# Kernel optimization log

Hardware: AMD Instinct MI355X
Metric: run time of the kernel (lower is better)

The kernel has to match this reference:

```python
import jax, jax.numpy as jnp
import numpy as np

B, S, D = 8, 4096, 768
HEADS = 12
NEIGHBORS = 2
DILATION = 1
KERNEL = 1 + 2 * NEIGHBORS  # 5
DIM_HEAD = D // HEADS


def setup_inputs() -> dict:
    key = jax.random.key(0)
    ks = jax.random.split(key, 11)
    sc = 1.0 / np.sqrt(D)
    return {
        "x": jax.random.normal(ks[0], (B, S, D), dtype=jnp.float32),
        "Wq": jax.random.normal(ks[1], (D, D), dtype=jnp.float32) * sc,
        "bq": jax.random.normal(ks[2], (D,), dtype=jnp.float32) * 0.02,
        "Wk": jax.random.normal(ks[3], (D, D), dtype=jnp.float32) * sc,
        "bk": jax.random.normal(ks[4], (D,), dtype=jnp.float32) * 0.02,
        "Wv": jax.random.normal(ks[5], (D, D), dtype=jnp.float32) * sc,
        "bv": jax.random.normal(ks[6], (D,), dtype=jnp.float32) * 0.02,
        "Wo": jax.random.normal(ks[7], (D, D), dtype=jnp.float32) * sc,
        "bo": jax.random.normal(ks[8], (D,), dtype=jnp.float32) * 0.02,
        "gamma": jnp.ones((D,), dtype=jnp.float32),
        "beta": jnp.zeros((D,), dtype=jnp.float32),
    }


def _extract_seq_patches(x, kernel_size, dilation):
    # [B, S, D] -> [B, S, kernel_size, D] of dilated local windows, zero-padded.
    seq_len = x.shape[1]
    patch_size = kernel_size + (dilation - 1) * (kernel_size - 1)
    pad_r = (patch_size - 1) // 2
    pad_l = patch_size - pad_r - 1
    xp = jnp.pad(x, ((0, 0), (pad_l, pad_r), (0, 0)))
    # small fixed loop over kernel positions (kernel_size = 5)
    return jnp.stack([xp[:, i:i + seq_len] for i in range(0, patch_size, dilation)], axis=2)


def reference(x, Wq, bq, Wk, bk, Wv, bv, Wo, bo, gamma, beta):
    patches = _extract_seq_patches(x, KERNEL, DILATION)  # [B, S, K, D]
    q = x @ Wq + bq                                       # [B, S, D]
    k = patches @ Wk + bk                                 # [B, S, K, D]
    v = patches @ Wv + bv                                 # [B, S, K, D]
    # split heads
    q = q.reshape(B, S, HEADS, DIM_HEAD)
    k = k.reshape(B, S, KERNEL, HEADS, DIM_HEAD)
    v = v.reshape(B, S, KERNEL, HEADS, DIM_HEAD)
    scale = jnp.sqrt(jnp.asarray(DIM_HEAD, dtype=q.dtype))
    scores = jnp.einsum('bshd,bskhd->bshk', q, k) / scale  # [B, S, H, K]
    p = jax.nn.softmax(scores, axis=-1)
    att = jnp.einsum('bshk,bskhd->bshd', p, v)             # [B, S, H, dh]
    att = att.reshape(B, S, D)
    att = att @ Wo + bo
    y = att + x
    # LayerNorm over last dim
    mu = jnp.mean(y, axis=-1, keepdims=True)
    var = jnp.var(y, axis=-1, keepdims=True)
    y = (y - mu) / jnp.sqrt(var + 1e-5) * gamma + beta
    return y
```

## Files before the change

### kernel.cpp

```cpp
#include <hip/hip_runtime.h>

#define B_  8
#define S_  4096
#define D_  768
#define H_  12
#define M_  (B_ * S_)
#define NQKV_ 2304
#define NTILES 12

typedef unsigned short u16;
typedef __attribute__((ext_vector_type(4))) float  f32x4;
typedef __attribute__((ext_vector_type(8))) __bf16 bf16x8;
typedef __attribute__((ext_vector_type(4))) u16    u16x4;

#define GAS __attribute__((address_space(1)))
#define LAS __attribute__((address_space(3)))

__device__ __forceinline__ u16 f2bf(float f) {
    unsigned u = __float_as_uint(f);
    u += 0x7FFF + ((u >> 16) & 1);
    return (u16)(u >> 16);
}
__device__ __forceinline__ float bf2f(u16 h) {
    return __uint_as_float(((unsigned)h) << 16);
}

__device__ __forceinline__ void gload_lds16(const void* g, void* l) {
    __builtin_amdgcn_global_load_lds((const GAS void*)g, (LAS void*)l, 16, 0, 0);
}

__device__ __forceinline__ int xcd_swz(int bid, int nwg) {
    return (bid & 7) * (nwg >> 3) + (bid >> 3);
}

__global__ __launch_bounds__(256) void castx_kernel(const float* __restrict__ x,
                                                    u16* __restrict__ xb) {
    const int i = blockIdx.x * 256 + threadIdx.x;
    const float4 v = ((const float4*)x)[i];
    u16x4 o;
    o.x = f2bf(v.x); o.y = f2bf(v.y); o.z = f2bf(v.z); o.w = f2bf(v.w);
    ((u16x4*)xb)[i] = o;
}

__global__ __launch_bounds__(256) void wtrans_kernel(const float* __restrict__ Wq,
                                                     const float* __restrict__ Wk,
                                                     const float* __restrict__ Wv,
                                                     const float* __restrict__ Wo,
                                                     u16* __restrict__ Wb) {
    const float* W = (blockIdx.z == 0) ? Wq : (blockIdx.z == 1) ? Wk
                   : (blockIdx.z == 2) ? Wv : Wo;
    u16* O = Wb + (size_t)blockIdx.z * D_ * D_;
    __shared__ float tile[32][33];
    const int tx = threadIdx.x & 31, ty = threadIdx.x >> 5;
    const int k0 = blockIdx.y * 32, n0 = blockIdx.x * 32;
#pragma unroll
    for (int j = 0; j < 4; j++)
        tile[ty + j * 8][tx] = W[(size_t)(k0 + ty + j * 8) * D_ + n0 + tx];
    __syncthreads();
#pragma unroll
    for (int j = 0; j < 4; j++)
        O[(size_t)(n0 + ty + j * 8) * D_ + k0 + tx] = f2bf(tile[tx][ty + j * 8]);
}


#define MFMA16(AF, BF)                                                       \
    __builtin_amdgcn_s_setprio(1);                                           \
    _Pragma("unroll") for (int mi = 0; mi < 4; ++mi)                         \
        _Pragma("unroll") for (int ni = 0; ni < 4; ++ni)                     \
            acc[mi][ni] = __builtin_amdgcn_mfma_f32_16x16x32_bf16(           \
                AF[mi], BF[ni], acc[mi][ni], 0, 0, 0);                       \
    __builtin_amdgcn_s_setprio(0)

#define RD(p, imm) (*(const bf16x8*)((p) + (imm)))

template <int MODE>
__global__ __launch_bounds__(256, 2) void gemm2_kernel(
    const u16* __restrict__ A, const u16* __restrict__ Wb,
    const float* __restrict__ b0, const float* __restrict__ b1,
    const float* __restrict__ b2,
    u16* __restrict__ outb, const u16* __restrict__ xres) {
    extern __shared__ char lds[];

    const int t = threadIdx.x;
    const int w = t >> 6, l = t & 63;
    const int wm = w >> 1, wn = w & 1;

    const int NTN = (MODE == 0) ? 18 : 6;
    const int work = xcd_swz(blockIdx.x, gridDim.x);
    const int mt = work / NTN, nt = work % NTN;
    const int m0 = mt * 128;
    const int col0 = nt * 128;
    const int widx = (MODE == 0) ? (nt / 6) : 3;
    const int n0w  = (MODE == 0) ? (nt % 6) * 128 : col0;

    const int srow = w * 32 + (l >> 3);
    const int schunk = (l & 7) ^ ((l >> 3) & 7);
    const u16* Asrc = A + (size_t)(m0 + srow) * D_ + schunk * 8;
    const u16* Bsrc = Wb + (size_t)widx * (D_ * D_)
                         + (size_t)(n0w + srow) * D_ + schunk * 8;
    char* const dstA = lds + w * 4096;
    char* const dstB = lds + 16384 + w * 4096;

    const int ck0 = (((l >> 4) ^ (l & 7)) << 4);
    const int ck1 = ((((l >> 4) + 4) ^ (l & 7)) << 4);
    const char* aB = lds + (wm * 64 + (l & 15)) * 128;
    const char* bB = lds + 16384 + (wn * 64 + (l & 15)) * 128;

    f32x4 acc[4][4];
#pragma unroll
    for (int i = 0; i < 4; i++)
#pragma unroll
        for (int j = 0; j < 4; j++) acc[i][j] = (f32x4){0.f, 0.f, 0.f, 0.f};

    auto STAGE = [&](int tk, int b) {
        const int ko = tk * 64;
        char* da = dstA + b * 32768;
        char* db = dstB + b * 32768;
#pragma unroll
        for (int g = 0; g < 4; ++g) {
            gload_lds16(Asrc + ko + g * 8 * D_, da + g * 1024);
            gload_lds16(Bsrc + ko + g * 8 * D_, db + g * 1024);
        }
    };

    STAGE(0, 0);
    __syncthreads();

#pragma unroll
    for (int X = 0; X < NTILES; ++X) {
        const int cb = (X & 1) * 32768;
        if (X + 1 < NTILES) STAGE(X + 1, (X & 1) ^ 1);

        bf16x8 af[4], bf[4];
#pragma unroll
        for (int mi = 0; mi < 4; ++mi) af[mi] = RD(aB, cb + mi * 2048 + ck0);
#pragma unroll
        for (int ni = 0; ni < 4; ++ni) bf[ni] = RD(bB, cb + ni * 2048 + ck0);
        MFMA16(af, bf);
#pragma unroll
        for (int mi = 0; mi < 4; ++mi) af[mi] = RD(aB, cb + mi * 2048 + ck1);
#pragma unroll
        for (int ni = 0; ni < 4; ++ni) bf[ni] = RD(bB, cb + ni * 2048 + ck1);
        MFMA16(af, bf);

        __syncthreads();
    }

    const int crow0 = m0 + wm * 64 + ((l >> 4) << 2);
    const int ccol0 = col0 + wn * 64 + (l & 15);
    if (MODE == 0) {
        const float* bias = (widx == 0) ? b0 : (widx == 1) ? b1 : b2;
        const int bcol0 = ccol0 - widx * D_;
#pragma unroll
        for (int mi = 0; mi < 4; ++mi)
#pragma unroll
            for (int ni = 0; ni < 4; ++ni) {
                const float bv = bias[bcol0 + ni * 16];
#pragma unroll
                for (int r = 0; r < 4; ++r)
                    outb[(size_t)(crow0 + mi * 16 + r) * NQKV_ + ccol0 + ni * 16] =
                        f2bf(acc[mi][ni][r] + bv);
            }
    } else {
#pragma unroll
        for (int mi = 0; mi < 4; ++mi)
#pragma unroll
            for (int ni = 0; ni < 4; ++ni) {
                const int col = ccol0 + ni * 16;
                const float bv = b0[col];
#pragma unroll
                for (int r = 0; r < 4; ++r) {
                    const size_t idx = (size_t)(crow0 + mi * 16 + r) * D_ + col;
                    outb[idx] = f2bf(acc[mi][ni][r] + bv + bf2f(xres[idx]));
                }
            }
    }
}

__global__ __launch_bounds__(256) void attn_kernel(const u16* __restrict__ QKV,
                                                   const float* __restrict__ bk,
                                                   const float* __restrict__ bv,
                                                   u16* __restrict__ att) {
    const int gw = xcd_swz(blockIdx.x, gridDim.x) * 4 + (threadIdx.x >> 6);
    const int l  = threadIdx.x & 63;
    const int hq = gw % 3;
    const int m  = gw / 3;
    const int s  = m & (S_ - 1);
    const int col = hq * 256 + l * 4;
    const u16* base = QKV + (size_t)m * NQKV_;

    const u16x4 qv = *(const u16x4*)(base + col);
    float qf[4];
#pragma unroll
    for (int j = 0; j < 4; j++) qf[j] = bf2f(qv[j]);

    float sc[5];
#pragma unroll
    for (int i = 0; i < 5; i++) {
        const int sp = s + i - 2;
        float p;
        if (sp >= 0 && sp < S_) {
            const u16x4 kv = *(const u16x4*)(base + (i - 2) * NQKV_ + D_ + col);
            p = qf[0] * bf2f(kv[0]) + qf[1] * bf2f(kv[1])
              + qf[2] * bf2f(kv[2]) + qf[3] * bf2f(kv[3]);
        } else {
            const float4 kb = *(const float4*)(bk + col);
            p = qf[0] * kb.x + qf[1] * kb.y + qf[2] * kb.z + qf[3] * kb.w;
        }
#pragma unroll
        for (int off = 1; off < 16; off <<= 1) p += __shfl_xor(p, off, 64);
        sc[i] = p * 0.125f;
    }
    float mx = sc[0];
#pragma unroll
    for (int i = 1; i < 5; i++) mx = fmaxf(mx, sc[i]);
    float e[5], sum = 0.f;
#pragma unroll
    for (int i = 0; i < 5; i++) { e[i] = __expf(sc[i] - mx); sum += e[i]; }
    const float inv = 1.f / sum;

    float o[4] = {0.f, 0.f, 0.f, 0.f};
#pragma unroll
    for (int i = 0; i < 5; i++) {
        const float wgt = e[i] * inv;
        const int sp = s + i - 2;
        if (sp >= 0 && sp < S_) {
            const u16x4 vv = *(const u16x4*)(base + (i - 2) * NQKV_ + 2 * D_ + col);
#pragma unroll
            for (int j = 0; j < 4; j++) o[j] += wgt * bf2f(vv[j]);
        } else {
            const float4 vb = *(const float4*)(bv + col);
            o[0] += wgt * vb.x; o[1] += wgt * vb.y;
            o[2] += wgt * vb.z; o[3] += wgt * vb.w;
        }
    }
    u16x4 ov;
#pragma unroll
    for (int j = 0; j < 4; j++) ov[j] = f2bf(o[j]);
    *(u16x4*)(att + (size_t)m * D_ + col) = ov;
}

__global__ __launch_bounds__(256) void ln_kernel(const u16* __restrict__ Yb,
                                                 const float* __restrict__ gamma,
                                                 const float* __restrict__ beta,
                                                 float* __restrict__ out) {
    const int row = blockIdx.x;
    const u16* r = Yb + (size_t)row * D_;
    const int t = threadIdx.x;
    const float v0 = bf2f(r[t]), v1 = bf2f(r[t + 256]), v2 = bf2f(r[t + 512]);
    float s  = v0 + v1 + v2;
    float s2 = v0 * v0 + v1 * v1 + v2 * v2;
#pragma unroll
    for (int off = 32; off > 0; off >>= 1) {
        s  += __shfl_xor(s,  off, 64);
        s2 += __shfl_xor(s2, off, 64);
    }
    __shared__ float red[8];
    const int w = t >> 6, l = t & 63;
    if (l == 0) { red[w] = s; red[4 + w] = s2; }
    __syncthreads();
    s  = red[0] + red[1] + red[2] + red[3];
    s2 = red[4] + red[5] + red[6] + red[7];
    const float mu  = s * (1.f / 768.f);
    const float var = s2 * (1.f / 768.f) - mu * mu;
    const float inv = rsqrtf(var + 1e-5f);
    float* o = out + (size_t)row * D_;
    o[t]       = (v0 - mu) * inv * gamma[t]       + beta[t];
    o[t + 256] = (v1 - mu) * inv * gamma[t + 256] + beta[t + 256];
    o[t + 512] = (v2 - mu) * inv * gamma[t + 512] + beta[t + 512];
}

extern "C" void kernel_launch(void* const* d_in, const int* in_sizes, int n_in,
                              void* d_out, int out_size, void* d_ws, size_t ws_size,
                              hipStream_t stream) {
    const float* x     = (const float*)d_in[0];
    const float* Wq    = (const float*)d_in[1];
    const float* bq    = (const float*)d_in[2];
    const float* Wk    = (const float*)d_in[3];
    const float* bk    = (const float*)d_in[4];
    const float* Wv    = (const float*)d_in[5];
    const float* bv    = (const float*)d_in[6];
    const float* Wo    = (const float*)d_in[7];
    const float* bo    = (const float*)d_in[8];
    const float* gamma = (const float*)d_in[9];
    const float* beta  = (const float*)d_in[10];

    char* ws = (char*)d_ws;
    u16*   Wb  = (u16*)ws;
    u16*   xb  = (u16*)(ws + 4718592);
    u16*   QKV = (u16*)(ws + 4718592 + 50331648);
    u16*   yb  = QKV;
    u16*   att = (u16*)d_out;

    (void)hipFuncSetAttribute(reinterpret_cast<const void*>(&gemm2_kernel<0>),
                              hipFuncAttributeMaxDynamicSharedMemorySize, 65536);
    (void)hipFuncSetAttribute(reinterpret_cast<const void*>(&gemm2_kernel<1>),
                              hipFuncAttributeMaxDynamicSharedMemorySize, 65536);

    castx_kernel<<<(M_ * D_) / (256 * 4), 256, 0, stream>>>(x, xb);
    wtrans_kernel<<<dim3(24, 24, 4), 256, 0, stream>>>(Wq, Wk, Wv, Wo, Wb);
    gemm2_kernel<0><<<(M_ / 128) * 18, 256, 65536, stream>>>(xb, Wb, bq, bk, bv,
                                                             QKV, nullptr);
    attn_kernel<<<(M_ * 3) / 4, 256, 0, stream>>>(QKV, bk, bv, att);
    gemm2_kernel<1><<<(M_ / 128) * 6, 256, 65536, stream>>>(att, Wb, bo, nullptr, nullptr,
                                                            yb, xb);
    ln_kernel<<<M_, 256, 0, stream>>>(yb, gamma, beta, (float*)d_out);
}
```

Before: 291.8 us.

## Replace LDS-staged GEMM with register-direct global loads and 64x64 per-wave tiles

Both GEMMs stop staging A and B tiles through double-buffered LDS with global_load_lds. Each wave now loads its MFMA fragments straight from global memory into registers, using two register buffers that alternate. The block tile changes from 128x128 (2x2 waves) to 64x256: each wave owns a 64x64 output tile and shares the A rows with the other waves only through cache. This removes LDS traffic and block barriers, but gives up cross-wave reuse, so global and L2 traffic per FLOP goes up and register pressure rises.

```diff
diff --git a/kernel.cpp b/kernel.cpp
--- a/kernel.cpp
+++ b/kernel.cpp
@@ -13,9 +13,6 @@
 typedef __attribute__((ext_vector_type(8))) __bf16 bf16x8;
 typedef __attribute__((ext_vector_type(4))) u16    u16x4;
 
-#define GAS __attribute__((address_space(1)))
-#define LAS __attribute__((address_space(3)))
-
 __device__ __forceinline__ u16 f2bf(float f) {
     unsigned u = __float_as_uint(f);
     u += 0x7FFF + ((u >> 16) & 1);
@@ -23,10 +20,6 @@
 }
 __device__ __forceinline__ float bf2f(u16 h) {
     return __uint_as_float(((unsigned)h) << 16);
-}
-
-__device__ __forceinline__ void gload_lds16(const void* g, void* l) {
-    __builtin_amdgcn_global_load_lds((const GAS void*)g, (LAS void*)l, 16, 0, 0);
 }
 
 __device__ __forceinline__ int xcd_swz(int bid, int nwg) {
@@ -63,48 +56,48 @@
 }
 
 
-#define MFMA16(AF, BF)                                                       \
+#define RDG(p, off) (*(const bf16x8*)((p) + (off)))
+
+#define LOADT(FA, FB, kt)                                                    \
+    _Pragma("unroll") for (int mi = 0; mi < 4; ++mi)                         \
+        _Pragma("unroll") for (int kh = 0; kh < 2; ++kh)                     \
+            FA[mi][kh] = RDG(Ap, (size_t)mi * 16 * D_ + (kt) * 64 + kh * 32); \
+    _Pragma("unroll") for (int ni = 0; ni < 4; ++ni)                         \
+        _Pragma("unroll") for (int kh = 0; kh < 2; ++kh)                     \
+            FB[ni][kh] = RDG(Bp, (size_t)ni * 16 * D_ + (kt) * 64 + kh * 32)
+
+#define MFMA_ALL(FA, FB)                                                     \
     __builtin_amdgcn_s_setprio(1);                                           \
-    _Pragma("unroll") for (int mi = 0; mi < 4; ++mi)                         \
-        _Pragma("unroll") for (int ni = 0; ni < 4; ++ni)                     \
-            acc[mi][ni] = __builtin_amdgcn_mfma_f32_16x16x32_bf16(           \
-                AF[mi], BF[ni], acc[mi][ni], 0, 0, 0);                       \
+    _Pragma("unroll") for (int kh = 0; kh < 2; ++kh)                         \
+        _Pragma("unroll") for (int mi = 0; mi < 4; ++mi)                     \
+            _Pragma("unroll") for (int ni = 0; ni < 4; ++ni)                 \
+                acc[mi][ni] = __builtin_amdgcn_mfma_f32_16x16x32_bf16(       \
+                    FA[mi][kh], FB[ni][kh], acc[mi][ni], 0, 0, 0);           \
     __builtin_amdgcn_s_setprio(0)
 
-#define RD(p, imm) (*(const bf16x8*)((p) + (imm)))
-
 template <int MODE>
-__global__ __launch_bounds__(256, 2) void gemm2_kernel(
+__global__ __launch_bounds__(256) void gemmr_kernel(
     const u16* __restrict__ A, const u16* __restrict__ Wb,
-    const float* __restrict__ b0, const float* __restrict__ b1,
-    const float* __restrict__ b2,
+    const float* __restrict__ bq, const float* __restrict__ bk,
+    const float* __restrict__ bv,
     u16* __restrict__ outb, const u16* __restrict__ xres) {
-    extern __shared__ char lds[];
-
     const int t = threadIdx.x;
     const int w = t >> 6, l = t & 63;
-    const int wm = w >> 1, wn = w & 1;
-
-    const int NTN = (MODE == 0) ? 18 : 6;
-    const int work = xcd_swz(blockIdx.x, gridDim.x);
-    const int mt = work / NTN, nt = work % NTN;
-    const int m0 = mt * 128;
-    const int col0 = nt * 128;
-    const int widx = (MODE == 0) ? (nt / 6) : 3;
-    const int n0w  = (MODE == 0) ? (nt % 6) * 128 : col0;
-
-    const int srow = w * 32 + (l >> 3);
-    const int schunk = (l & 7) ^ ((l >> 3) & 7);
-    const u16* Asrc = A + (size_t)(m0 + srow) * D_ + schunk * 8;
-    const u16* Bsrc = Wb + (size_t)widx * (D_ * D_)
-                         + (size_t)(n0w + srow) * D_ + schunk * 8;
-    char* const dstA = lds + w * 4096;
-    char* const dstB = lds + 16384 + w * 4096;
-
-    const int ck0 = (((l >> 4) ^ (l & 7)) << 4);
-    const int ck1 = ((((l >> 4) + 4) ^ (l & 7)) << 4);
-    const char* aB = lds + (wm * 64 + (l & 15)) * 128;
-    const char* bB = lds + 16384 + (wn * 64 + (l & 15)) * 128;
+
+    const int NTB = (MODE == 0) ? 9 : 3;
+    const int bw = xcd_swz(blockIdx.x, gridDim.x);
+    const int mt = bw / NTB, ng = bw % NTB;
+    const int m0 = mt * 64;
+    const int nt = ng * 4 + w;
+    const int col0 = nt * 64;
+    const int widx = (MODE == 0) ? (col0 / D_) : 3;
+    const int n0w  = col0 - ((MODE == 0) ? widx * D_ : 0);
+
+    const int fr = l & 15;
+    const int kg = l >> 4;
+    const u16* Ap = A + (size_t)(m0 + fr) * D_ + kg * 8;
+    const u16* Bp = Wb + (size_t)widx * (D_ * D_)
+                       + (size_t)(n0w + fr) * D_ + kg * 8;
 
     f32x4 acc[4][4];
 #pragma unroll
@@ -112,54 +105,31 @@
 #pragma unroll
         for (int j = 0; j < 4; j++) acc[i][j] = (f32x4){0.f, 0.f, 0.f, 0.f};
 
-    auto STAGE = [&](int tk, int b) {
-        const int ko = tk * 64;
-        char* da = dstA + b * 32768;
-        char* db = dstB + b * 32768;
-#pragma unroll
-        for (int g = 0; g < 4; ++g) {
-            gload_lds16(Asrc + ko + g * 8 * D_, da + g * 1024);
-            gload_lds16(Bsrc + ko + g * 8 * D_, db + g * 1024);
-        }
-    };
-
-    STAGE(0, 0);
-    __syncthreads();
-
-#pragma unroll
-    for (int X = 0; X < NTILES; ++X) {
-        const int cb = (X & 1) * 32768;
-        if (X + 1 < NTILES) STAGE(X + 1, (X & 1) ^ 1);
-
-        bf16x8 af[4], bf[4];
-#pragma unroll
-        for (int mi = 0; mi < 4; ++mi) af[mi] = RD(aB, cb + mi * 2048 + ck0);
-#pragma unroll
-        for (int ni = 0; ni < 4; ++ni) bf[ni] = RD(bB, cb + ni * 2048 + ck0);
-        MFMA16(af, bf);
-#pragma unroll
-        for (int mi = 0; mi < 4; ++mi) af[mi] = RD(aB, cb + mi * 2048 + ck1);
-#pragma unroll
-        for (int ni = 0; ni < 4; ++ni) bf[ni] = RD(bB, cb + ni * 2048 + ck1);
-        MFMA16(af, bf);
-
-        __syncthreads();
-    }
-
-    const int crow0 = m0 + wm * 64 + ((l >> 4) << 2);
-    const int ccol0 = col0 + wn * 64 + (l & 15);
+    bf16x8 Af0[4][2], Bf0[4][2], Af1[4][2], Bf1[4][2];
+
+    LOADT(Af0, Bf0, 0);
+#pragma unroll
+    for (int kt = 0; kt < NTILES; kt += 2) {
+        LOADT(Af1, Bf1, kt + 1);
+        MFMA_ALL(Af0, Bf0);
+        if (kt + 2 < NTILES) LOADT(Af0, Bf0, kt + 2);
+        MFMA_ALL(Af1, Bf1);
+    }
+
+    const int crow0 = m0 + ((l >> 4) << 2);
+    const int ccol0 = col0 + fr;
     if (MODE == 0) {
-        const float* bias = (widx == 0) ? b0 : (widx == 1) ? b1 : b2;
+        const float* bias = (widx == 0) ? bq : (widx == 1) ? bk : bv;
         const int bcol0 = ccol0 - widx * D_;
 #pragma unroll
         for (int mi = 0; mi < 4; ++mi)
 #pragma unroll
             for (int ni = 0; ni < 4; ++ni) {
-                const float bv = bias[bcol0 + ni * 16];
+                const float bv_ = bias[bcol0 + ni * 16];
 #pragma unroll
                 for (int r = 0; r < 4; ++r)
                     outb[(size_t)(crow0 + mi * 16 + r) * NQKV_ + ccol0 + ni * 16] =
-                        f2bf(acc[mi][ni][r] + bv);
+                        f2bf(acc[mi][ni][r] + bv_);
             }
     } else {
 #pragma unroll
@@ -167,11 +137,11 @@
 #pragma unroll
             for (int ni = 0; ni < 4; ++ni) {
                 const int col = ccol0 + ni * 16;
-                const float bv = b0[col];
+                const float bv_ = bq[col];
 #pragma unroll
                 for (int r = 0; r < 4; ++r) {
                     const size_t idx = (size_t)(crow0 + mi * 16 + r) * D_ + col;
-                    outb[idx] = f2bf(acc[mi][ni][r] + bv + bf2f(xres[idx]));
+                    outb[idx] = f2bf(acc[mi][ni][r] + bv_ + bf2f(xres[idx]));
                 }
             }
     }
@@ -292,17 +262,12 @@
     u16*   yb  = QKV;
     u16*   att = (u16*)d_out;
 
-    (void)hipFuncSetAttribute(reinterpret_cast<const void*>(&gemm2_kernel<0>),
-                              hipFuncAttributeMaxDynamicSharedMemorySize, 65536);
-    (void)hipFuncSetAttribute(reinterpret_cast<const void*>(&gemm2_kernel<1>),
-                              hipFuncAttributeMaxDynamicSharedMemorySize, 65536);
-
     castx_kernel<<<(M_ * D_) / (256 * 4), 256, 0, stream>>>(x, xb);
     wtrans_kernel<<<dim3(24, 24, 4), 256, 0, stream>>>(Wq, Wk, Wv, Wo, Wb);
-    gemm2_kernel<0><<<(M_ / 128) * 18, 256, 65536, stream>>>(xb, Wb, bq, bk, bv,
-                                                             QKV, nullptr);
+    gemmr_kernel<0><<<(M_ / 64) * 9, 256, 0, stream>>>(xb, Wb, bq, bk, bv,
+                                                       QKV, nullptr);
     attn_kernel<<<(M_ * 3) / 4, 256, 0, stream>>>(QKV, bk, bv, att);
-    gemm2_kernel<1><<<(M_ / 128) * 6, 256, 65536, stream>>>(att, Wb, bo, nullptr, nullptr,
-                                                            yb, xb);
+    gemmr_kernel<1><<<(M_ / 64) * 3, 256, 0, stream>>>(att, Wb, bo, nullptr, nullptr,
+                                                       yb, xb);
     ln_kernel<<<M_, 256, 0, stream>>>(yb, gamma, beta, (float*)d_out);
 }
```

Result: slower. 639.9 us (+119.3%).
